# Kernel optimization log

Hardware: AMD Instinct MI355X
Metric: run time of the kernel (lower is better)

## Reference

```python
import jax, jax.numpy as jnp
import numpy as np

NVEC = [100000, 100000, 100000]
OFFSETS = np.concatenate([[0], np.cumsum(NVEC)[:-1]]).astype(np.int32)  # [0,100000,200000]
DIM = 64
B = 500000
HID = 50
IN_DIM = len(NVEC) * DIM + 1  # 193


def setup_inputs() -> dict:
    key = jax.random.key(0)
    ks = jax.random.split(key, 7)
    batch_ind = jax.random.randint(ks[0], (B, len(NVEC)), 0, NVEC[0], dtype=jnp.int32)
    batch_t = jax.random.uniform(ks[1], (B,), dtype=jnp.float32)
    U = jax.random.uniform(ks[2], (int(np.sum(NVEC)), DIM), dtype=jnp.float32)
    W1 = jax.random.normal(ks[3], (IN_DIM, HID), dtype=jnp.float32) * 0.1
    b1 = jax.random.normal(ks[4], (HID,), dtype=jnp.float32) * 0.1
    W2 = jax.random.normal(ks[5], (HID, 1), dtype=jnp.float32) * 0.1
    b2 = jax.random.normal(ks[6], (1,), dtype=jnp.float32) * 0.1
    return {"batch_ind": batch_ind, "batch_t": batch_t, "U": U,
            "W1": W1, "b1": b1, "W2": W2, "b2": b2}


def reference(batch_ind, batch_t, U, W1, b1, W2, b2):
    # per-mode gather: offset each mode's index into the concatenated U table
    offs = jnp.asarray(OFFSETS)  # [nmod]
    idx = batch_ind + offs[None, :]          # [B, nmod] global row ids
    emb = U[idx]                              # [B, nmod, D] single fused gather
    X = jnp.concatenate([emb.reshape(emb.shape[0], -1),
                         batch_t[:, None]], axis=1)  # [B, nmod*D+1]
    h = jnp.tanh(X @ W1 + b1)                 # [B, 50]
    return h @ W2 + b2                        # [B, 1]
```

## Files before the change

### kernel.cpp

```cpp
#include <hip/hip_runtime.h>
#include <hip/hip_bf16.h>

using bf16x8 = __attribute__((ext_vector_type(8))) short;
using f32x4  = __attribute__((ext_vector_type(4))) float;

#define THREADS 256
#define NBLOCKS 768
#define NTILES  31250
#define UELEMS  19200000
#define WS_NEED (UELEMS * 2)

__device__ __forceinline__ short f2bf(float f) {
    __hip_bfloat16 h = __float2bfloat16(f);
    return __builtin_bit_cast(short, h);
}

__device__ __forceinline__ bf16x8 cvt8(float4 a, float4 b) {
    bf16x8 r;
    r[0] = f2bf(a.x); r[1] = f2bf(a.y); r[2] = f2bf(a.z); r[3] = f2bf(a.w);
    r[4] = f2bf(b.x); r[5] = f2bf(b.y); r[6] = f2bf(b.z); r[7] = f2bf(b.w);
    return r;
}

__global__ __launch_bounds__(256) void cvtU_kernel(const float* __restrict__ U,
                                                   short* __restrict__ Ub) {
    const int stride = gridDim.x * blockDim.x;
    for (int i = blockIdx.x * blockDim.x + threadIdx.x; i < UELEMS / 8; i += stride) {
        float4 a = ((const float4*)U)[2 * i];
        float4 b = ((const float4*)U)[2 * i + 1];
        ((bf16x8*)Ub)[i] = cvt8(a, b);
    }
}

template <bool BF16PATH>
__global__ __launch_bounds__(THREADS) void etl_kernel(
    const int*   __restrict__ bi,
    const float* __restrict__ t,
    const float* __restrict__ U,
    const short* __restrict__ Ub,
    const float* __restrict__ W1,
    const float* __restrict__ b1,
    const float* __restrict__ W2,
    const float* __restrict__ b2,
    float*       __restrict__ out)
{
    __shared__ short bsh[24][64][8];
    for (int e = threadIdx.x; e < 24 * 64; e += THREADS) {
        int f = e >> 6, l = e & 63;
        int nt = f / 6, ks = f - nt * 6;
        int n  = nt * 16 + (l & 15);
        int k0 = ks * 32 + ((l >> 4) << 3);
        bf16x8 v;
#pragma unroll
        for (int j = 0; j < 8; ++j) {
            float w = (n < 50) ? W1[(k0 + j) * 50 + n] : 0.f;
            v[j] = f2bf(w);
        }
        *(bf16x8*)(&bsh[f][l][0]) = v;
    }
    __syncthreads();

    const int lane = threadIdx.x & 63;
    const int g    = lane >> 4;
    const int ncol = lane & 15;

    bf16x8 Bf[24];
#pragma unroll
    for (int f = 0; f < 24; ++f) Bf[f] = *(const bf16x8*)(&bsh[f][lane][0]);

    float w192[4], b1r[4], w2r[4];
#pragma unroll
    for (int nt = 0; nt < 4; ++nt) {
        int n = nt * 16 + ncol;
        bool vld = (n < 50);
        w192[nt] = vld ? W1[192 * 50 + n] : 0.f;
        b1r[nt]  = vld ? b1[n] : 0.f;
        w2r[nt]  = vld ? W2[n] : 0.f;
    }
    const float b2v = b2[0];

    const int nwaves = NBLOCKS * (THREADS / 64);
    const int wid    = blockIdx.x * (THREADS / 64) + (threadIdx.x >> 6);

    for (int tile = wid; tile < NTILES; tile += nwaves) {
        const int base = tile * 16;
        const int row  = base + ncol;

        int i0 = bi[row * 3 + 0];
        int i1 = bi[row * 3 + 1] + 100000;
        int i2 = bi[row * 3 + 2] + 200000;

        bf16x8 A[6];
        if constexpr (BF16PATH) {
            const short* q0 = Ub + (size_t)i0 * 64 + g * 8;
            const short* q1 = Ub + (size_t)i1 * 64 + g * 8;
            const short* q2 = Ub + (size_t)i2 * 64 + g * 8;
            A[0] = *(const bf16x8*)q0;  A[1] = *(const bf16x8*)(q0 + 32);
            A[2] = *(const bf16x8*)q1;  A[3] = *(const bf16x8*)(q1 + 32);
            A[4] = *(const bf16x8*)q2;  A[5] = *(const bf16x8*)(q2 + 32);
        } else {
            const float* p0 = U + (size_t)i0 * 64 + g * 8;
            const float* p1 = U + (size_t)i1 * 64 + g * 8;
            const float* p2 = U + (size_t)i2 * 64 + g * 8;
            float4 a0 = ((const float4*)p0)[0],        a1 = ((const float4*)p0)[1];
            float4 a2 = ((const float4*)(p0 + 32))[0], a3 = ((const float4*)(p0 + 32))[1];
            float4 b0 = ((const float4*)p1)[0],        b1v4 = ((const float4*)p1)[1];
            float4 b2v4 = ((const float4*)(p1 + 32))[0], b3 = ((const float4*)(p1 + 32))[1];
            float4 c0 = ((const float4*)p2)[0],        c1 = ((const float4*)p2)[1];
            float4 c2 = ((const float4*)(p2 + 32))[0], c3 = ((const float4*)(p2 + 32))[1];
            A[0] = cvt8(a0, a1);   A[1] = cvt8(a2, a3);
            A[2] = cvt8(b0, b1v4); A[3] = cvt8(b2v4, b3);
            A[4] = cvt8(c0, c1);   A[5] = cvt8(c2, c3);
        }

        f32x4 acc[4];
#pragma unroll
        for (int nt = 0; nt < 4; ++nt) acc[nt] = (f32x4){0.f, 0.f, 0.f, 0.f};
#pragma unroll
        for (int ks = 0; ks < 6; ++ks) {
#pragma unroll
            for (int nt = 0; nt < 4; ++nt) {
                acc[nt] = __builtin_amdgcn_mfma_f32_16x16x32_bf16(
                    A[ks], Bf[nt * 6 + ks], acc[nt], 0, 0, 0);
            }
        }

        float4 tv = *(const float4*)(t + base + g * 4);
        float tarr[4] = {tv.x, tv.y, tv.z, tv.w};
        float part[4] = {0.f, 0.f, 0.f, 0.f};
#pragma unroll
        for (int nt = 0; nt < 4; ++nt) {
#pragma unroll
            for (int r = 0; r < 4; ++r) {
                float pre = acc[nt][r] + tarr[r] * w192[nt] + b1r[nt];
                float e  = __expf(2.f * pre);
                float h  = 1.f - 2.f * __builtin_amdgcn_rcpf(e + 1.f);
                part[r] += h * w2r[nt];
            }
        }
#pragma unroll
        for (int r = 0; r < 4; ++r) {
#pragma unroll
            for (int m = 1; m < 16; m <<= 1)
                part[r] += __shfl_xor(part[r], m, 64);
        }
        if (ncol == 0) {
            float4 o = make_float4(part[0] + b2v, part[1] + b2v,
                                   part[2] + b2v, part[3] + b2v);
            *(float4*)(out + base + g * 4) = o;
        }
    }
}

extern "C" void kernel_launch(void* const* d_in, const int* in_sizes, int n_in,
                              void* d_out, int out_size, void* d_ws, size_t ws_size,
                              hipStream_t stream) {
    const int*   bi = (const int*)  d_in[0];
    const float* t  = (const float*)d_in[1];
    const float* U  = (const float*)d_in[2];
    const float* W1 = (const float*)d_in[3];
    const float* b1 = (const float*)d_in[4];
    const float* W2 = (const float*)d_in[5];
    const float* b2 = (const float*)d_in[6];
    float* out = (float*)d_out;

    if (ws_size >= (size_t)WS_NEED) {
        short* Ub = (short*)d_ws;
        cvtU_kernel<<<2048, 256, 0, stream>>>(U, Ub);
        etl_kernel<true><<<NBLOCKS, THREADS, 0, stream>>>(
            bi, t, U, Ub, W1, b1, W2, b2, out);
    } else {
        etl_kernel<false><<<NBLOCKS, THREADS, 0, stream>>>(
            bi, t, U, (const short*)nullptr, W1, b1, W2, b2, out);
    }
}
```

Baseline: 62.78 us.

## Pipeline bf16 embedding gathers through LDS with async global_load_lds prefetch

Rewrites the bf16 path so each wave gathers the next tile's embedding rows straight into a per-wave LDS buffer with global_load_lds. These loads overlap with the MFMA and tanh work on the current tile. Indices and time values are prefetched two tiles ahead, and an XOR swizzle is meant to avoid LDS bank conflicts when the fragments are read back. The cost is more LDS use, explicit waitcnt and sched_barrier fencing, and a fixed iteration count that clamps out-of-range tiles to redundant loads.

```diff
diff --git a/kernel.cpp b/kernel.cpp
--- a/kernel.cpp
+++ b/kernel.cpp
@@ -6,7 +6,9 @@
 
 #define THREADS 256
 #define NBLOCKS 768
+#define NWAVES  (NBLOCKS * (THREADS / 64))
 #define NTILES  31250
+#define NITER   11
 #define UELEMS  19200000
 #define WS_NEED (UELEMS * 2)
 
@@ -20,6 +22,12 @@
     r[0] = f2bf(a.x); r[1] = f2bf(a.y); r[2] = f2bf(a.z); r[3] = f2bf(a.w);
     r[4] = f2bf(b.x); r[5] = f2bf(b.y); r[6] = f2bf(b.z); r[7] = f2bf(b.w);
     return r;
+}
+
+__device__ __forceinline__ void glds16(const short* g, short* l) {
+    __builtin_amdgcn_global_load_lds(
+        (const __attribute__((address_space(1))) void*)g,
+        (__attribute__((address_space(3))) void*)l, 16, 0, 0);
 }
 
 __global__ __launch_bounds__(256) void cvtU_kernel(const float* __restrict__ U,
@@ -32,12 +40,159 @@
     }
 }
 
-template <bool BF16PATH>
-__global__ __launch_bounds__(THREADS) void etl_kernel(
+__global__ __launch_bounds__(THREADS) void etl_bf16(
+    const int*   __restrict__ bi,
+    const float* __restrict__ t,
+    const short* __restrict__ Ub,
+    const float* __restrict__ W1,
+    const float* __restrict__ b1,
+    const float* __restrict__ W2,
+    const float* __restrict__ b2,
+    float*       __restrict__ out)
+{
+    __shared__ short bsh[24][64][8];
+    __shared__ __align__(16) short gbuf[4][3072];
+
+    for (int e = threadIdx.x; e < 24 * 64; e += THREADS) {
+        int f = e >> 6, l = e & 63;
+        int nt = f / 6, ks = f - nt * 6;
+        int n  = nt * 16 + (l & 15);
+        int k0 = ks * 32 + ((l >> 4) << 3);
+        bf16x8 v;
+#pragma unroll
+        for (int j = 0; j < 8; ++j) {
+            float w = (n < 50) ? W1[(k0 + j) * 50 + n] : 0.f;
+            v[j] = f2bf(w);
+        }
+        *(bf16x8*)(&bsh[f][l][0]) = v;
+    }
+    __syncthreads();
+
+    const int lane = threadIdx.x & 63;
+    const int g    = lane >> 4;
+    const int ncol = lane & 15;
+    const int warp = threadIdx.x >> 6;
+    short* buf = &gbuf[warp][0];
+
+    bf16x8 Bf[24];
+#pragma unroll
+    for (int f = 0; f < 24; ++f) Bf[f] = *(const bf16x8*)(&bsh[f][lane][0]);
+
+    float w192[4], b1r[4], w2r[4];
+#pragma unroll
+    for (int nt = 0; nt < 4; ++nt) {
+        int n = nt * 16 + ncol;
+        bool vld = (n < 50);
+        w192[nt] = vld ? W1[192 * 50 + n] : 0.f;
+        b1r[nt]  = vld ? b1[n] : 0.f;
+        w2r[nt]  = vld ? W2[n] : 0.f;
+    }
+    const float b2v = b2[0];
+
+    const int wid = blockIdx.x * (THREADS / 64) + warp;
+
+    auto tileAt = [&](int i) {
+        int tl = wid + i * NWAVES;
+        return tl < NTILES ? tl : NTILES - 1;
+    };
+    auto loadIdx = [&](int i) -> int {
+        int m = lane >> 4; if (m > 2) m = 2;
+        int r = tileAt(i) * 16 + (lane & 15);
+        return bi[r * 3 + m] + m * 100000;
+    };
+    auto issueGather = [&](int idxv) {
+#pragma unroll
+        for (int j = 0; j < 6; ++j) {
+            int rr    = 8 * j + (lane >> 3);
+            int rowid = __shfl(idxv, rr, 64);
+            const short* gp = Ub + (size_t)rowid * 64
+                              + (((lane & 7) ^ (lane >> 3)) << 3);
+            glds16(gp, buf + j * 512);
+        }
+    };
+    auto readFrags = [&](bf16x8* A) {
+#pragma unroll
+        for (int ks = 0; ks < 6; ++ks) {
+            int mode = ks >> 1, h = ks & 1;
+            int off  = (mode * 16 + ncol) * 64
+                     + ((((h << 2) + g) ^ (lane & 7)) << 3);
+            A[ks] = *(const bf16x8*)(buf + off);
+        }
+    };
+
+    bf16x8 A[6];
+    int   idxv = loadIdx(0);
+    issueGather(idxv);
+    int   idx_n = loadIdx(1);
+    float4 tcur = *(const float4*)(t + tileAt(0) * 16 + g * 4);
+
+    asm volatile("s_waitcnt vmcnt(0)" ::: "memory");
+    __builtin_amdgcn_sched_barrier(0);
+    readFrags(A);
+    asm volatile("s_waitcnt lgkmcnt(0)" ::: "memory");
+    __builtin_amdgcn_sched_barrier(0);
+    issueGather(idx_n);
+    int   idx_n2 = loadIdx(2);
+    float4 tN = *(const float4*)(t + tileAt(1) * 16 + g * 4);
+
+    for (int i = 0; i < NITER; ++i) {
+        const int  tl    = wid + i * NWAVES;
+        const bool valid = tl < NTILES;
+        const int  base  = (valid ? tl : NTILES - 1) * 16;
+
+        f32x4 acc[4];
+#pragma unroll
+        for (int nt = 0; nt < 4; ++nt) acc[nt] = (f32x4){0.f, 0.f, 0.f, 0.f};
+#pragma unroll
+        for (int ks = 0; ks < 6; ++ks) {
+#pragma unroll
+            for (int nt = 0; nt < 4; ++nt) {
+                acc[nt] = __builtin_amdgcn_mfma_f32_16x16x32_bf16(
+                    A[ks], Bf[nt * 6 + ks], acc[nt], 0, 0, 0);
+            }
+        }
+
+        float tarr[4] = {tcur.x, tcur.y, tcur.z, tcur.w};
+        float part[4] = {0.f, 0.f, 0.f, 0.f};
+#pragma unroll
+        for (int nt = 0; nt < 4; ++nt) {
+#pragma unroll
+            for (int r = 0; r < 4; ++r) {
+                float pre = acc[nt][r] + tarr[r] * w192[nt] + b1r[nt];
+                float e  = __expf(2.f * pre);
+                float h  = 1.f - 2.f * __builtin_amdgcn_rcpf(e + 1.f);
+                part[r] += h * w2r[nt];
+            }
+        }
+#pragma unroll
+        for (int r = 0; r < 4; ++r) {
+#pragma unroll
+            for (int m = 1; m < 16; m <<= 1)
+                part[r] += __shfl_xor(part[r], m, 64);
+        }
+        const bool doStore = valid && (ncol == 0);
+        float4 o = make_float4(part[0] + b2v, part[1] + b2v,
+                               part[2] + b2v, part[3] + b2v);
+
+        asm volatile("s_waitcnt vmcnt(0)" ::: "memory");
+        __builtin_amdgcn_sched_barrier(0);
+        readFrags(A);
+        asm volatile("s_waitcnt lgkmcnt(0)" ::: "memory");
+        __builtin_amdgcn_sched_barrier(0);
+        issueGather(idx_n2);
+        idx_n2 = loadIdx(i + 3);
+        tcur = tN;
+        tN = *(const float4*)(t + tileAt(i + 2) * 16 + g * 4);
+
+        if (doStore)
+            *(float4*)(out + base + g * 4) = o;
+    }
+}
+
+__global__ __launch_bounds__(THREADS) void etl_f32(
     const int*   __restrict__ bi,
     const float* __restrict__ t,
     const float* __restrict__ U,
-    const short* __restrict__ Ub,
     const float* __restrict__ W1,
     const float* __restrict__ b1,
     const float* __restrict__ W2,
@@ -85,33 +240,20 @@
     for (int tile = wid; tile < NTILES; tile += nwaves) {
         const int base = tile * 16;
         const int row  = base + ncol;
-
         int i0 = bi[row * 3 + 0];
         int i1 = bi[row * 3 + 1] + 100000;
         int i2 = bi[row * 3 + 2] + 200000;
 
         bf16x8 A[6];
-        if constexpr (BF16PATH) {
-            const short* q0 = Ub + (size_t)i0 * 64 + g * 8;
-            const short* q1 = Ub + (size_t)i1 * 64 + g * 8;
-            const short* q2 = Ub + (size_t)i2 * 64 + g * 8;
-            A[0] = *(const bf16x8*)q0;  A[1] = *(const bf16x8*)(q0 + 32);
-            A[2] = *(const bf16x8*)q1;  A[3] = *(const bf16x8*)(q1 + 32);
-            A[4] = *(const bf16x8*)q2;  A[5] = *(const bf16x8*)(q2 + 32);
-        } else {
-            const float* p0 = U + (size_t)i0 * 64 + g * 8;
-            const float* p1 = U + (size_t)i1 * 64 + g * 8;
-            const float* p2 = U + (size_t)i2 * 64 + g * 8;
-            float4 a0 = ((const float4*)p0)[0],        a1 = ((const float4*)p0)[1];
-            float4 a2 = ((const float4*)(p0 + 32))[0], a3 = ((const float4*)(p0 + 32))[1];
-            float4 b0 = ((const float4*)p1)[0],        b1v4 = ((const float4*)p1)[1];
-            float4 b2v4 = ((const float4*)(p1 + 32))[0], b3 = ((const float4*)(p1 + 32))[1];
-            float4 c0 = ((const float4*)p2)[0],        c1 = ((const float4*)p2)[1];
-            float4 c2 = ((const float4*)(p2 + 32))[0], c3 = ((const float4*)(p2 + 32))[1];
-            A[0] = cvt8(a0, a1);   A[1] = cvt8(a2, a3);
-            A[2] = cvt8(b0, b1v4); A[3] = cvt8(b2v4, b3);
-            A[4] = cvt8(c0, c1);   A[5] = cvt8(c2, c3);
-        }
+        const float* p0 = U + (size_t)i0 * 64 + g * 8;
+        const float* p1 = U + (size_t)i1 * 64 + g * 8;
+        const float* p2 = U + (size_t)i2 * 64 + g * 8;
+        A[0] = cvt8(((const float4*)p0)[0], ((const float4*)p0)[1]);
+        A[1] = cvt8(((const float4*)(p0 + 32))[0], ((const float4*)(p0 + 32))[1]);
+        A[2] = cvt8(((const float4*)p1)[0], ((const float4*)p1)[1]);
+        A[3] = cvt8(((const float4*)(p1 + 32))[0], ((const float4*)(p1 + 32))[1]);
+        A[4] = cvt8(((const float4*)p2)[0], ((const float4*)p2)[1]);
+        A[5] = cvt8(((const float4*)(p2 + 32))[0], ((const float4*)(p2 + 32))[1]);
 
         f32x4 acc[4];
 #pragma unroll
@@ -167,10 +309,8 @@
     if (ws_size >= (size_t)WS_NEED) {
         short* Ub = (short*)d_ws;
         cvtU_kernel<<<2048, 256, 0, stream>>>(U, Ub);
-        etl_kernel<true><<<NBLOCKS, THREADS, 0, stream>>>(
-            bi, t, U, Ub, W1, b1, W2, b2, out);
+        etl_bf16<<<NBLOCKS, THREADS, 0, stream>>>(bi, t, Ub, W1, b1, W2, b2, out);
     } else {
-        etl_kernel<false><<<NBLOCKS, THREADS, 0, stream>>>(
-            bi, t, U, (const short*)nullptr, W1, b1, W2, b2, out);
-    }
-}
+        etl_f32<<<NBLOCKS, THREADS, 0, stream>>>(bi, t, U, W1, b1, W2, b2, out);
+    }
+}
```

Result: slower. 77.28 us (+23.1%).
